# Kernel tuning notes

Hardware: AMD Instinct MI355X
Metric: run time of the kernel (lower is better)

Reference implementation:

```python
import jax, jax.numpy as jnp
import numpy as np
from functools import partial

STRIDES = (8, 16, 32)
SCORE_THRESH = 0.3
NMS_THRESH = 0.5
TOPK = 500          # fixed pre-NMS candidate count (jit-friendly substitute for boolean masking)
CLASS_OFFSET = 1e4  # offset boxes per class so cross-class IoU == 0 -> per-class NMS


def _decode(cls, reg, obj, stride):
    # cls [B,C,H,W], reg [B,4,H,W], obj [B,1,H,W]
    B, C, H, W = cls.shape
    yv, xv = jnp.meshgrid(jnp.arange(H, dtype=cls.dtype), jnp.arange(W, dtype=cls.dtype), indexing='ij')
    scores = jax.nn.sigmoid(obj) * jax.nn.sigmoid(cls)          # [B,C,H,W]
    dx, dy, dw, dh = reg[:, 0], reg[:, 1], reg[:, 2], reg[:, 3]
    cx = (xv + jax.nn.sigmoid(dx)) * stride
    cy = (yv + jax.nn.sigmoid(dy)) * stride
    w = jnp.exp(dw) * stride
    h = jnp.exp(dh) * stride
    boxes = jnp.stack([cx - w / 2, cy - h / 2, cx + w / 2, cy + h / 2], axis=-1)  # [B,H,W,4]
    return boxes.reshape(B, H * W, 4), scores.reshape(B, C, H * W).transpose(0, 2, 1)


def _pairwise_iou(boxes):
    # boxes [B,K,4] xyxy -> iou [B,K,K]
    area = (boxes[..., 2] - boxes[..., 0]) * (boxes[..., 3] - boxes[..., 1])
    x1 = jnp.maximum(boxes[:, :, None, 0], boxes[:, None, :, 0])
    y1 = jnp.maximum(boxes[:, :, None, 1], boxes[:, None, :, 1])
    x2 = jnp.minimum(boxes[:, :, None, 2], boxes[:, None, :, 2])
    y2 = jnp.minimum(boxes[:, :, None, 3], boxes[:, None, :, 3])
    inter = jnp.clip(x2 - x1, 0) * jnp.clip(y2 - y1, 0)
    union = area[:, :, None] + area[:, None, :] - inter
    return inter / (union + 1e-7)


def _greedy_nms(iou, valid):
    # iou [B,K,K], valid [B,K] -> keep [B,K]; greedy over score-sorted order (axis 1)
    B, K = valid.shape
    def step(supp, i):
        keep_i = valid[:, i] & ~supp[:, i]                    # [B]
        supp = supp | (keep_i[:, None] & (iou[:, i, :] >= NMS_THRESH))
        return supp, keep_i
    _, keep_t = jax.lax.scan(step, jnp.zeros((B, K), dtype=bool), jnp.arange(K))
    return keep_t.T  # [B,K]


def _predict(levels):
    boxes_l, scores_l = [], []
    for (c, r, o), s in zip(levels, STRIDES):
        b, sc = _decode(c, r, o, s)
        boxes_l.append(b)
        scores_l.append(sc)
    boxes = jnp.concatenate(boxes_l, axis=1)     # [B,N,4]
    scores = jnp.concatenate(scores_l, axis=1)   # [B,N,C]
    max_scores = scores.max(axis=-1)             # [B,N]
    labels = jnp.argmax(scores, axis=-1)         # [B,N]
    masked = jnp.where(max_scores > SCORE_THRESH, max_scores, -1.0)
    top_scores, idx = jax.lax.top_k(masked, TOPK)                         # sorted desc
    top_boxes = jnp.take_along_axis(boxes, idx[..., None], axis=1)        # [B,K,4]
    top_labels = jnp.take_along_axis(labels, idx, axis=1)                 # [B,K]
    valid = top_scores > SCORE_THRESH
    boxes_off = top_boxes + (top_labels.astype(top_boxes.dtype) * CLASS_OFFSET)[..., None]
    keep = _greedy_nms(_pairwise_iou(boxes_off), valid)                   # [B,K]
    out_boxes = jnp.where(keep[..., None], top_boxes, 0.0)
    out_scores = jnp.where(keep, top_scores, 0.0)
    return out_boxes, out_scores, top_labels, keep


def setup_inputs() -> dict:
    key = jax.random.key(0)
    ks = jax.random.split(key, 9)
    B, C = 64, 2
    shapes = {
        'cls_p3': (B, C, 160, 160), 'reg_p3': (B, 4, 160, 160), 'obj_p3': (B, 1, 160, 160),
        'cls_p4': (B, C, 80, 80),   'reg_p4': (B, 4, 80, 80),   'obj_p4': (B, 1, 80, 80),
        'cls_p5': (B, C, 40, 40),   'reg_p5': (B, 4, 40, 40),   'obj_p5': (B, 1, 40, 40),
    }
    return {name: jax.random.normal(k, shp, dtype=jnp.float32)
            for k, (name, shp) in zip(ks, shapes.items())}


def reference(cls_p3, reg_p3, obj_p3, cls_p4, reg_p4, obj_p4, cls_p5, reg_p5, obj_p5):
    levels = [(cls_p3, reg_p3, obj_p3), (cls_p4, reg_p4, obj_p4), (cls_p5, reg_p5, obj_p5)]
    return _predict(levels)
```

## Files before the change

kernel.cpp:

```cpp
#include <hip/hip_runtime.h>
#include <hip/hip_bf16.h>
#include <stdint.h>

#define NB 64
#define NA 33600
#define NK 500
#define HW3 25600
#define HW4 6400
#define HW5 1600
#define OFF4 25600
#define OFF5 32000
#define NBIN 2048
#define CAP 2048
#define NA4 8400
#define MROWS 512

typedef unsigned int u32;
typedef unsigned long long u64;

__device__ __forceinline__ float sigf(float x) { return 1.0f / (1.0f + expf(-x)); }

__device__ __forceinline__ u32 f2key(float f) {
  u32 u = __float_as_uint(f);
  return (u & 0x80000000u) ? ~u : (u | 0x80000000u);
}
__device__ __forceinline__ float key2f(u32 k) {
  u32 u = (k & 0x80000000u) ? (k ^ 0x80000000u) : ~k;
  return __uint_as_float(u);
}
__device__ __forceinline__ int bin_of(float s) {
  int b = (int)(s * 2048.0f);
  return b > 2047 ? 2047 : b;
}
__device__ __forceinline__ u32 mkkey(float o, float c0, float c1) {
  float so = sigf(o);
  float s = fmaxf(so * sigf(c0), so * sigf(c1));
  float masked = (s > 0.3f) ? s : -1.0f;
  return f2key(masked);
}

__global__ __launch_bounds__(256) void k_score(
    const float* __restrict__ cls3, const float* __restrict__ obj3,
    const float* __restrict__ cls4, const float* __restrict__ obj4,
    const float* __restrict__ cls5, const float* __restrict__ obj5,
    uint4* __restrict__ keys4)
{
  int b = blockIdx.y;
  int i4 = blockIdx.x * 256 + threadIdx.x;
  if (i4 >= NA4) return;
  const float* cls; const float* obj; int p4, HW;
  if (i4 < 6400)      { cls = cls3; obj = obj3; p4 = i4;        HW = HW3; }
  else if (i4 < 8000) { cls = cls4; obj = obj4; p4 = i4 - 6400; HW = HW4; }
  else                { cls = cls5; obj = obj5; p4 = i4 - 8000; HW = HW5; }
  float4 o  = reinterpret_cast<const float4*>(obj + (size_t)b * HW)[p4];
  float4 c0 = reinterpret_cast<const float4*>(cls + (size_t)(b * 2) * HW)[p4];
  float4 c1 = reinterpret_cast<const float4*>(cls + (size_t)(b * 2 + 1) * HW)[p4];
  uint4 kv;
  kv.x = mkkey(o.x, c0.x, c1.x);
  kv.y = mkkey(o.y, c0.y, c1.y);
  kv.z = mkkey(o.z, c0.z, c1.z);
  kv.w = mkkey(o.w, c0.w, c1.w);
  keys4[(size_t)b * NA4 + i4] = kv;
}

__global__ __launch_bounds__(1024) void k_topk(
    const u32* __restrict__ keys, int* __restrict__ ok,
    int* __restrict__ top_idx, float* __restrict__ top_score)
{
  int b = blockIdx.x, tid = threadIdx.x;
  __shared__ u32 hist[NBIN];
  __shared__ u32 part[256];
  __shared__ u64 cand[CAP];
  __shared__ u32 lcnt;
  __shared__ int sh_p;
  for (int i = tid; i < NBIN; i += 1024) hist[i] = 0;
  if (tid == 0) lcnt = 0;
  __syncthreads();

  const uint4* kb4 = reinterpret_cast<const uint4*>(keys + (size_t)b * NA);
  for (int i4 = tid; i4 < NA4; i4 += 1024) {
    uint4 kv = kb4[i4];
    u32 ks[4] = {kv.x, kv.y, kv.z, kv.w};
#pragma unroll
    for (int c = 0; c < 4; ++c) {
      float s = key2f(ks[c]);
      if (s > 0.3f) atomicAdd(&hist[bin_of(s)], 1u);
    }
  }
  __syncthreads();
  if (tid < 256) {
    u32 s8 = 0;
#pragma unroll
    for (int k = 0; k < 8; ++k) s8 += hist[tid * 8 + k];
    part[tid] = s8;
  }
  __syncthreads();
  for (int off = 1; off < 256; off <<= 1) {
    u32 add = 0;
    if (tid < 256 && tid + off < 256) add = part[tid + off];
    __syncthreads();
    if (tid < 256) part[tid] += add;
    __syncthreads();
  }
  if (tid == 0 && part[0] < NK) sh_p = -1;
  if (tid < 256) {
    u32 S = part[tid];
    u32 Snext = (tid == 255) ? 0u : part[tid + 1];
    if (S >= NK && Snext < NK) {
      u32 run = Snext;
      int p = tid * 8;
      for (int k = 7; k >= 0; --k) {
        run += hist[tid * 8 + k];
        if (run >= NK) { p = tid * 8 + k; break; }
      }
      sh_p = p;
    }
  }
  __syncthreads();
  int p = sh_p;
  if (p < 0) { if (tid == 0) ok[b] = 0; return; }
  for (int i4 = tid; i4 < NA4; i4 += 1024) {
    uint4 kv = kb4[i4];
    u32 ks[4] = {kv.x, kv.y, kv.z, kv.w};
#pragma unroll
    for (int c = 0; c < 4; ++c) {
      float s = key2f(ks[c]);
      if (s > 0.3f && bin_of(s) >= p) {
        u32 slot = atomicAdd(&lcnt, 1u);
        if (slot < CAP) cand[slot] = ((u64)ks[c] << 16) | (u32)(0xFFFF - (i4 * 4 + c));
      }
    }
  }
  __syncthreads();
  if (lcnt > CAP) { if (tid == 0) ok[b] = 0; return; }
  if (tid == 0) ok[b] = 1;
  int n = (int)lcnt;
  for (int t = tid; t < n; t += 1024) {
    u64 k = cand[t];
    int rank = 0;
    for (int j = 0; j < n; ++j) rank += (cand[j] > k) ? 1 : 0;
    if (rank < NK) {
      top_idx[b * NK + rank]   = 0xFFFF - (int)(k & 0xFFFFull);
      top_score[b * NK + rank] = key2f((u32)(k >> 16));
    }
  }
}

__global__ __launch_bounds__(1024) void k_select_fb(
    const u32* __restrict__ keys, const int* __restrict__ ok,
    int* __restrict__ top_idx, float* __restrict__ top_score)
{
  int b = blockIdx.x;
  if (ok[b]) return;
  int tid = threadIdx.x;
  __shared__ u32 hist[256];
  __shared__ u32 suf[256];
  __shared__ u64 coll[512];
  __shared__ u32 sh_R;
  __shared__ int sh_digit;
  __shared__ u32 sh_cnt;
  const u32* kb = keys + (size_t)b * NA;
  if (tid == 0) sh_cnt = 0;

  u64 prefix = 0, prefmask = 0;
  u32 R = NK;
  for (int pass = 0; pass < 6; ++pass) {
    int shift = 40 - 8 * pass;
    if (tid < 256) hist[tid] = 0;
    __syncthreads();
    for (int i = tid; i < NA; i += 1024) {
      u64 k48 = ((u64)kb[i] << 16) | (u32)(0xFFFF - i);
      if ((k48 & prefmask) == prefix)
        atomicAdd(&hist[(u32)(k48 >> shift) & 255u], 1u);
    }
    __syncthreads();
    if (tid < 256) suf[tid] = hist[tid];
    __syncthreads();
    for (int off = 1; off < 256; off <<= 1) {
      u32 add = 0;
      if (tid < 256 && tid + off < 256) add = suf[tid + off];
      __syncthreads();
      if (tid < 256) suf[tid] += add;
      __syncthreads();
    }
    if (tid < 256) {
      u32 s = suf[tid];
      u32 snext = (tid == 255) ? 0u : suf[tid + 1];
      if (s >= R && snext < R) { sh_digit = tid; sh_R = R - snext; }
    }
    __syncthreads();
    int dsel = sh_digit;
    R = sh_R;
    prefix |= ((u64)dsel) << shift;
    prefmask |= 0xFFull << shift;
    __syncthreads();
  }

  for (int i = tid; i < NA; i += 1024) {
    u64 k48 = ((u64)kb[i] << 16) | (u32)(0xFFFF - i);
    if (k48 >= prefix) {
      u32 slot = atomicAdd(&sh_cnt, 1u);
      if (slot < 512) coll[slot] = k48;
    }
  }
  __syncthreads();
  int n = (sh_cnt < (u32)NK) ? (int)sh_cnt : NK;
  if (tid < NK) { top_idx[b * NK + tid] = 0; top_score[b * NK + tid] = -1.0f; }
  __syncthreads();
  for (int t = tid; t < n; t += 1024) {
    u64 k = coll[t];
    int rank = 0;
    for (int j = 0; j < n; ++j) rank += (coll[j] > k) ? 1 : 0;
    int idx = 0xFFFF - (int)(k & 0xFFFFull);
    top_idx[b * NK + rank] = idx;
    top_score[b * NK + rank] = key2f((u32)(k >> 16));
  }
}

__global__ __launch_bounds__(256) void k_decode(
    const int* __restrict__ top_idx,
    const float* __restrict__ cls3, const float* __restrict__ obj3, const float* __restrict__ reg3,
    const float* __restrict__ cls4, const float* __restrict__ obj4, const float* __restrict__ reg4,
    const float* __restrict__ cls5, const float* __restrict__ obj5, const float* __restrict__ reg5,
    float4* __restrict__ boxes, float4* __restrict__ boxesoff,
    float* __restrict__ out_labels)
{
  int t = blockIdx.x * 256 + threadIdx.x;
  if (t >= NB * NK) return;
  int b = t / NK;
  int a = top_idx[t];
  const float *cls, *obj, *reg; int pos, HW, x, y; float stride;
  if (a < OFF4) {
    cls = cls3; obj = obj3; reg = reg3; pos = a; HW = HW3; stride = 8.0f;
    y = pos / 160; x = pos - y * 160;
  } else if (a < OFF5) {
    cls = cls4; obj = obj4; reg = reg4; pos = a - OFF4; HW = HW4; stride = 16.0f;
    y = pos / 80; x = pos - y * 80;
  } else {
    cls = cls5; obj = obj5; reg = reg5; pos = a - OFF5; HW = HW5; stride = 32.0f;
    y = pos / 40; x = pos - y * 40;
  }
  float dx = reg[(b * 4 + 0) * HW + pos];
  float dy = reg[(b * 4 + 1) * HW + pos];
  float dw = reg[(b * 4 + 2) * HW + pos];
  float dh = reg[(b * 4 + 3) * HW + pos];
  float cx = ((float)x + sigf(dx)) * stride;
  float cy = ((float)y + sigf(dy)) * stride;
  float w = expf(dw) * stride;
  float h = expf(dh) * stride;
  float x1 = cx - w * 0.5f, y1 = cy - h * 0.5f;
  float x2 = cx + w * 0.5f, y2 = cy + h * 0.5f;
  float so = sigf(obj[b * HW + pos]);
  float s0 = so * sigf(cls[(b * 2) * HW + pos]);
  float s1 = so * sigf(cls[(b * 2 + 1) * HW + pos]);
  int label = (s1 > s0) ? 1 : 0;
  float off = (float)label * 10000.0f;
  boxes[t]    = make_float4(x1, y1, x2, y2);
  boxesoff[t] = make_float4(x1 + off, y1 + off, x2 + off, y2 + off);
  out_labels[t] = (float)label;
}

__global__ __launch_bounds__(256) void k_iou(
    const float4* __restrict__ boxesoff, u64* __restrict__ mask)
{
  int t = blockIdx.x * 256 + threadIdx.x;
  if (t >= NB * NK * 8) return;
  int w = t & 7;
  int bi = t >> 3;
  int b = bi / NK;
  int i = bi - b * NK;
  float4 A = boxesoff[bi];
  float areaA = (A.z - A.x) * (A.w - A.y);
  const float4* base = boxesoff + b * NK;
  int j0 = w * 64;
  int jmax = (NK - j0 < 64) ? (NK - j0) : 64;
  u64 bits = 0;
  for (int jj = 0; jj < jmax; ++jj) {
    float4 Bx = base[j0 + jj];
    float areaB = (Bx.z - Bx.x) * (Bx.w - Bx.y);
    float ix1 = fmaxf(A.x, Bx.x);
    float iy1 = fmaxf(A.y, Bx.y);
    float ix2 = fminf(A.z, Bx.z);
    float iy2 = fminf(A.w, Bx.w);
    float iw = fmaxf(ix2 - ix1, 0.0f);
    float ih = fmaxf(iy2 - iy1, 0.0f);
    float inter = iw * ih;
    float uni = areaA + areaB - inter;
    float iou = inter / (uni + 1e-7f);
    bits |= ((u64)(iou >= 0.5f)) << jj;
  }
  mask[(size_t)b * (MROWS * 8) + (size_t)i * 8 + w] = bits;
}

__global__ __launch_bounds__(64) void k_nms(
    const u64* __restrict__ mask, const float* __restrict__ top_score,
    const float4* __restrict__ boxes,
    float* __restrict__ out_boxes, float* __restrict__ out_scores,
    float* __restrict__ out_keep)
{
  int b = blockIdx.x;
  int lane = threadIdx.x;
  const u64* mb = mask + (size_t)b * (MROWS * 8);

  u64 validw[8];
#pragma unroll
  for (int c = 0; c < 8; ++c) {
    int r = c * 64 + lane;
    float s = (r < NK) ? top_score[b * NK + r] : -1.0f;
    validw[c] = __ballot(s > 0.3f);
  }

  u64 supp[8] = {0, 0, 0, 0, 0, 0, 0, 0};
  u64 keepw[8];
  u64 row[2][8];

  {
    const u64* rp = mb + (size_t)lane * 8;
#pragma unroll
    for (int w = 0; w < 8; ++w) row[0][w] = rp[w];
  }

#pragma unroll
  for (int c = 0; c < 8; ++c) {
    const int cur = c & 1, nxt = cur ^ 1;
    if (c < 7) {
      const u64* rp = mb + (size_t)((c + 1) * 64 + lane) * 8;
#pragma unroll
      for (int w = 0; w < 8; ++w)
        if (w >= c + 1) row[nxt][w] = rp[w];
    }
    u32 rlo = (u32)row[cur][c];
    u32 rhi = (u32)(row[cur][c] >> 32);
    u64 sw = supp[c], vw = validw[c], km = 0;
#pragma unroll 4
    for (int i = 0; i < 64; ++i) {
      u64 wi = ((u64)(u32)__builtin_amdgcn_readlane(rhi, i) << 32) |
               (u64)(u32)__builtin_amdgcn_readlane(rlo, i);
      u64 bit = 1ull << i;
      if ((vw & bit) && !(sw & bit)) { sw |= wi; km |= bit; }
    }
    keepw[c] = km;
    u64 sel = ((km >> lane) & 1ull) ? ~0ull : 0ull;
#pragma unroll
    for (int w = c + 1; w < 8; ++w) {
      u64 v = row[cur][w] & sel;
#pragma unroll
      for (int off = 1; off < 64; off <<= 1)
        v |= (u64)__shfl_xor((unsigned long long)v, off, 64);
      supp[w] |= v;
    }
  }

#pragma unroll
  for (int c = 0; c < 8; ++c) {
    int r = c * 64 + lane;
    if (r < NK) {
      int kp = (int)((keepw[c] >> lane) & 1ull);
      float4 bx = boxes[b * NK + r];
      float s = top_score[b * NK + r];
      float4 ob;
      ob.x = kp ? bx.x : 0.0f;
      ob.y = kp ? bx.y : 0.0f;
      ob.z = kp ? bx.z : 0.0f;
      ob.w = kp ? bx.w : 0.0f;
      reinterpret_cast<float4*>(out_boxes)[b * NK + r] = ob;
      out_scores[b * NK + r] = kp ? s : 0.0f;
      out_keep[b * NK + r]   = kp ? 1.0f : 0.0f;
    }
  }
}

extern "C" void kernel_launch(void* const* d_in, const int* in_sizes, int n_in,
                              void* d_out, int out_size, void* d_ws, size_t ws_size,
                              hipStream_t stream) {
  const float* cls3 = (const float*)d_in[0];
  const float* reg3 = (const float*)d_in[1];
  const float* obj3 = (const float*)d_in[2];
  const float* cls4 = (const float*)d_in[3];
  const float* reg4 = (const float*)d_in[4];
  const float* obj4 = (const float*)d_in[5];
  const float* cls5 = (const float*)d_in[6];
  const float* reg5 = (const float*)d_in[7];
  const float* obj5 = (const float*)d_in[8];

  char* ws = (char*)d_ws;
  u32*    keys      = (u32*)   (ws + 0);
  int*    ok        = (int*)   (ws + 8601600);
  int*    top_idx   = (int*)   (ws + 8601856);
  float*  top_score = (float*) (ws + 8729856);
  float4* boxes     = (float4*)(ws + 8857856);
  float4* boxesoff  = (float4*)(ws + 9369856);
  u64*    mask      = (u64*)   (ws + 9881856);

  float* out        = (float*)d_out;
  float* out_boxes  = out;
  float* out_scores = out + 128000;
  float* out_labels = out + 160000;
  float* out_keep   = out + 192000;

  dim3 gscore((NA4 + 255) / 256, NB);
  k_score<<<gscore, 256, 0, stream>>>(cls3, obj3, cls4, obj4, cls5, obj5, (uint4*)keys);
  k_topk<<<NB, 1024, 0, stream>>>(keys, ok, top_idx, top_score);
  k_select_fb<<<NB, 1024, 0, stream>>>(keys, ok, top_idx, top_score);
  k_decode<<<(NB * NK + 255) / 256, 256, 0, stream>>>(top_idx,
      cls3, obj3, reg3, cls4, obj4, reg4, cls5, obj5, reg5,
      boxes, boxesoff, out_labels);
  k_iou<<<(NB * NK * 8 + 255) / 256, 256, 0, stream>>>(boxesoff, mask);
  k_nms<<<NB, 64, 0, stream>>>(mask, top_score, boxes, out_boxes, out_scores, out_keep);
}
```

Measured before the change: 106.9 us.

## Fuse top-k, fallback selection and box decode into one kernel

Merges the top-k kernel, the radix-select fallback kernel and the decode kernel into a single per-batch block. Selected indices now stay in shared memory instead of going through global memory, and the ok flag goes away. This removes two launches and their global round trips. It also fully unrolls the NMS greedy inner loop and broadcasts the suppression word with readfirstlane so it stays in scalar registers. In exchange, decode runs on only 500 threads of a 64-block grid, which gives less parallelism for that part.

```diff
diff --git a/kernel.cpp b/kernel.cpp
--- a/kernel.cpp
+++ b/kernel.cpp
@@ -37,6 +37,11 @@
   float s = fmaxf(so * sigf(c0), so * sigf(c1));
   float masked = (s > 0.3f) ? s : -1.0f;
   return f2key(masked);
+}
+__device__ __forceinline__ u64 uniform64(u64 v) {
+  u32 lo = (u32)__builtin_amdgcn_readfirstlane((int)(u32)v);
+  u32 hi = (u32)__builtin_amdgcn_readfirstlane((int)(u32)(v >> 32));
+  return ((u64)hi << 32) | lo;
 }
 
 __global__ __launch_bounds__(256) void k_score(
@@ -64,20 +69,33 @@
 }
 
 __global__ __launch_bounds__(1024) void k_topk(
-    const u32* __restrict__ keys, int* __restrict__ ok,
-    int* __restrict__ top_idx, float* __restrict__ top_score)
+    const u32* __restrict__ keys,
+    const float* __restrict__ cls3, const float* __restrict__ obj3, const float* __restrict__ reg3,
+    const float* __restrict__ cls4, const float* __restrict__ obj4, const float* __restrict__ reg4,
+    const float* __restrict__ cls5, const float* __restrict__ obj5, const float* __restrict__ reg5,
+    float* __restrict__ top_score,
+    float4* __restrict__ boxes, float4* __restrict__ boxesoff,
+    float* __restrict__ out_labels)
 {
   int b = blockIdx.x, tid = threadIdx.x;
   __shared__ u32 hist[NBIN];
   __shared__ u32 part[256];
   __shared__ u64 cand[CAP];
+  __shared__ int idx_lds[NK];
   __shared__ u32 lcnt;
   __shared__ int sh_p;
+  __shared__ u32 sh_R;
+  __shared__ int sh_digit;
+  __shared__ u32 sh_cnt;
+
   for (int i = tid; i < NBIN; i += 1024) hist[i] = 0;
-  if (tid == 0) lcnt = 0;
+  if (tid < NK) idx_lds[tid] = 0;
+  if (tid == 0) { lcnt = 0; }
   __syncthreads();
 
-  const uint4* kb4 = reinterpret_cast<const uint4*>(keys + (size_t)b * NA);
+  const u32* kb = keys + (size_t)b * NA;
+  const uint4* kb4 = reinterpret_cast<const uint4*>(kb);
+
   for (int i4 = tid; i4 < NA4; i4 += 1024) {
     uint4 kv = kb4[i4];
     u32 ks[4] = {kv.x, kv.y, kv.z, kv.w};
@@ -118,146 +136,125 @@
   }
   __syncthreads();
   int p = sh_p;
-  if (p < 0) { if (tid == 0) ok[b] = 0; return; }
-  for (int i4 = tid; i4 < NA4; i4 += 1024) {
-    uint4 kv = kb4[i4];
-    u32 ks[4] = {kv.x, kv.y, kv.z, kv.w};
-#pragma unroll
-    for (int c = 0; c < 4; ++c) {
-      float s = key2f(ks[c]);
-      if (s > 0.3f && bin_of(s) >= p) {
-        u32 slot = atomicAdd(&lcnt, 1u);
-        if (slot < CAP) cand[slot] = ((u64)ks[c] << 16) | (u32)(0xFFFF - (i4 * 4 + c));
-      }
-    }
-  }
-  __syncthreads();
-  if (lcnt > CAP) { if (tid == 0) ok[b] = 0; return; }
-  if (tid == 0) ok[b] = 1;
-  int n = (int)lcnt;
-  for (int t = tid; t < n; t += 1024) {
-    u64 k = cand[t];
-    int rank = 0;
-    for (int j = 0; j < n; ++j) rank += (cand[j] > k) ? 1 : 0;
-    if (rank < NK) {
-      top_idx[b * NK + rank]   = 0xFFFF - (int)(k & 0xFFFFull);
-      top_score[b * NK + rank] = key2f((u32)(k >> 16));
-    }
-  }
-}
-
-__global__ __launch_bounds__(1024) void k_select_fb(
-    const u32* __restrict__ keys, const int* __restrict__ ok,
-    int* __restrict__ top_idx, float* __restrict__ top_score)
-{
-  int b = blockIdx.x;
-  if (ok[b]) return;
-  int tid = threadIdx.x;
-  __shared__ u32 hist[256];
-  __shared__ u32 suf[256];
-  __shared__ u64 coll[512];
-  __shared__ u32 sh_R;
-  __shared__ int sh_digit;
-  __shared__ u32 sh_cnt;
-  const u32* kb = keys + (size_t)b * NA;
-  if (tid == 0) sh_cnt = 0;
-
-  u64 prefix = 0, prefmask = 0;
-  u32 R = NK;
-  for (int pass = 0; pass < 6; ++pass) {
-    int shift = 40 - 8 * pass;
-    if (tid < 256) hist[tid] = 0;
+  bool fail = (p < 0);
+  if (!fail) {
+    for (int i4 = tid; i4 < NA4; i4 += 1024) {
+      uint4 kv = kb4[i4];
+      u32 ks[4] = {kv.x, kv.y, kv.z, kv.w};
+#pragma unroll
+      for (int c = 0; c < 4; ++c) {
+        float s = key2f(ks[c]);
+        if (s > 0.3f && bin_of(s) >= p) {
+          u32 slot = atomicAdd(&lcnt, 1u);
+          if (slot < CAP) cand[slot] = ((u64)ks[c] << 16) | (u32)(0xFFFF - (i4 * 4 + c));
+        }
+      }
+    }
+    __syncthreads();
+    fail = (lcnt > CAP);
+  }
+
+  if (!fail) {
+    int n = (int)lcnt;
+    for (int t = tid; t < n; t += 1024) {
+      u64 k = cand[t];
+      int rank = 0;
+      for (int j = 0; j < n; ++j) rank += (cand[j] > k) ? 1 : 0;
+      if (rank < NK) {
+        idx_lds[rank] = 0xFFFF - (int)(k & 0xFFFFull);
+        top_score[b * NK + rank] = key2f((u32)(k >> 16));
+      }
+    }
+  } else {
+    u64 prefix = 0, prefmask = 0;
+    u32 R = NK;
+    for (int pass = 0; pass < 6; ++pass) {
+      int shift = 40 - 8 * pass;
+      if (tid < 256) part[tid] = 0;
+      __syncthreads();
+      for (int i = tid; i < NA; i += 1024) {
+        u64 k48 = ((u64)kb[i] << 16) | (u32)(0xFFFF - i);
+        if ((k48 & prefmask) == prefix)
+          atomicAdd(&part[(u32)(k48 >> shift) & 255u], 1u);
+      }
+      __syncthreads();
+      if (tid < 256) hist[tid] = part[tid];
+      __syncthreads();
+      for (int off = 1; off < 256; off <<= 1) {
+        u32 add = 0;
+        if (tid < 256 && tid + off < 256) add = hist[tid + off];
+        __syncthreads();
+        if (tid < 256) hist[tid] += add;
+        __syncthreads();
+      }
+      if (tid < 256) {
+        u32 s = hist[tid];
+        u32 snext = (tid == 255) ? 0u : hist[tid + 1];
+        if (s >= R && snext < R) { sh_digit = tid; sh_R = R - snext; }
+      }
+      __syncthreads();
+      prefix |= ((u64)sh_digit) << shift;
+      R = sh_R;
+      prefmask |= 0xFFull << shift;
+      __syncthreads();
+    }
+    if (tid == 0) sh_cnt = 0;
+    if (tid < NK) top_score[b * NK + tid] = -1.0f;
     __syncthreads();
     for (int i = tid; i < NA; i += 1024) {
       u64 k48 = ((u64)kb[i] << 16) | (u32)(0xFFFF - i);
-      if ((k48 & prefmask) == prefix)
-        atomicAdd(&hist[(u32)(k48 >> shift) & 255u], 1u);
+      if (k48 >= prefix) {
+        u32 slot = atomicAdd(&sh_cnt, 1u);
+        if (slot < 512) cand[slot] = k48;
+      }
     }
     __syncthreads();
-    if (tid < 256) suf[tid] = hist[tid];
-    __syncthreads();
-    for (int off = 1; off < 256; off <<= 1) {
-      u32 add = 0;
-      if (tid < 256 && tid + off < 256) add = suf[tid + off];
-      __syncthreads();
-      if (tid < 256) suf[tid] += add;
-      __syncthreads();
-    }
-    if (tid < 256) {
-      u32 s = suf[tid];
-      u32 snext = (tid == 255) ? 0u : suf[tid + 1];
-      if (s >= R && snext < R) { sh_digit = tid; sh_R = R - snext; }
-    }
-    __syncthreads();
-    int dsel = sh_digit;
-    R = sh_R;
-    prefix |= ((u64)dsel) << shift;
-    prefmask |= 0xFFull << shift;
-    __syncthreads();
-  }
-
-  for (int i = tid; i < NA; i += 1024) {
-    u64 k48 = ((u64)kb[i] << 16) | (u32)(0xFFFF - i);
-    if (k48 >= prefix) {
-      u32 slot = atomicAdd(&sh_cnt, 1u);
-      if (slot < 512) coll[slot] = k48;
+    int n = (sh_cnt < (u32)NK) ? (int)sh_cnt : NK;
+    for (int t = tid; t < n; t += 1024) {
+      u64 k = cand[t];
+      int rank = 0;
+      for (int j = 0; j < n; ++j) rank += (cand[j] > k) ? 1 : 0;
+      if (rank < NK) {
+        idx_lds[rank] = 0xFFFF - (int)(k & 0xFFFFull);
+        top_score[b * NK + rank] = key2f((u32)(k >> 16));
+      }
     }
   }
   __syncthreads();
-  int n = (sh_cnt < (u32)NK) ? (int)sh_cnt : NK;
-  if (tid < NK) { top_idx[b * NK + tid] = 0; top_score[b * NK + tid] = -1.0f; }
-  __syncthreads();
-  for (int t = tid; t < n; t += 1024) {
-    u64 k = coll[t];
-    int rank = 0;
-    for (int j = 0; j < n; ++j) rank += (coll[j] > k) ? 1 : 0;
-    int idx = 0xFFFF - (int)(k & 0xFFFFull);
-    top_idx[b * NK + rank] = idx;
-    top_score[b * NK + rank] = key2f((u32)(k >> 16));
-  }
-}
-
-__global__ __launch_bounds__(256) void k_decode(
-    const int* __restrict__ top_idx,
-    const float* __restrict__ cls3, const float* __restrict__ obj3, const float* __restrict__ reg3,
-    const float* __restrict__ cls4, const float* __restrict__ obj4, const float* __restrict__ reg4,
-    const float* __restrict__ cls5, const float* __restrict__ obj5, const float* __restrict__ reg5,
-    float4* __restrict__ boxes, float4* __restrict__ boxesoff,
-    float* __restrict__ out_labels)
-{
-  int t = blockIdx.x * 256 + threadIdx.x;
-  if (t >= NB * NK) return;
-  int b = t / NK;
-  int a = top_idx[t];
-  const float *cls, *obj, *reg; int pos, HW, x, y; float stride;
-  if (a < OFF4) {
-    cls = cls3; obj = obj3; reg = reg3; pos = a; HW = HW3; stride = 8.0f;
-    y = pos / 160; x = pos - y * 160;
-  } else if (a < OFF5) {
-    cls = cls4; obj = obj4; reg = reg4; pos = a - OFF4; HW = HW4; stride = 16.0f;
-    y = pos / 80; x = pos - y * 80;
-  } else {
-    cls = cls5; obj = obj5; reg = reg5; pos = a - OFF5; HW = HW5; stride = 32.0f;
-    y = pos / 40; x = pos - y * 40;
-  }
-  float dx = reg[(b * 4 + 0) * HW + pos];
-  float dy = reg[(b * 4 + 1) * HW + pos];
-  float dw = reg[(b * 4 + 2) * HW + pos];
-  float dh = reg[(b * 4 + 3) * HW + pos];
-  float cx = ((float)x + sigf(dx)) * stride;
-  float cy = ((float)y + sigf(dy)) * stride;
-  float w = expf(dw) * stride;
-  float h = expf(dh) * stride;
-  float x1 = cx - w * 0.5f, y1 = cy - h * 0.5f;
-  float x2 = cx + w * 0.5f, y2 = cy + h * 0.5f;
-  float so = sigf(obj[b * HW + pos]);
-  float s0 = so * sigf(cls[(b * 2) * HW + pos]);
-  float s1 = so * sigf(cls[(b * 2 + 1) * HW + pos]);
-  int label = (s1 > s0) ? 1 : 0;
-  float off = (float)label * 10000.0f;
-  boxes[t]    = make_float4(x1, y1, x2, y2);
-  boxesoff[t] = make_float4(x1 + off, y1 + off, x2 + off, y2 + off);
-  out_labels[t] = (float)label;
+
+  if (tid < NK) {
+    int a = idx_lds[tid];
+    const float *cls, *obj, *reg; int pos, HW, x, y; float stride;
+    if (a < OFF4) {
+      cls = cls3; obj = obj3; reg = reg3; pos = a; HW = HW3; stride = 8.0f;
+      y = pos / 160; x = pos - y * 160;
+    } else if (a < OFF5) {
+      cls = cls4; obj = obj4; reg = reg4; pos = a - OFF4; HW = HW4; stride = 16.0f;
+      y = pos / 80; x = pos - y * 80;
+    } else {
+      cls = cls5; obj = obj5; reg = reg5; pos = a - OFF5; HW = HW5; stride = 32.0f;
+      y = pos / 40; x = pos - y * 40;
+    }
+    float dx = reg[(b * 4 + 0) * HW + pos];
+    float dy = reg[(b * 4 + 1) * HW + pos];
+    float dw = reg[(b * 4 + 2) * HW + pos];
+    float dh = reg[(b * 4 + 3) * HW + pos];
+    float cx = ((float)x + sigf(dx)) * stride;
+    float cy = ((float)y + sigf(dy)) * stride;
+    float w = expf(dw) * stride;
+    float h = expf(dh) * stride;
+    float x1 = cx - w * 0.5f, y1 = cy - h * 0.5f;
+    float x2 = cx + w * 0.5f, y2 = cy + h * 0.5f;
+    float so = sigf(obj[b * HW + pos]);
+    float s0 = so * sigf(cls[(b * 2) * HW + pos]);
+    float s1 = so * sigf(cls[(b * 2 + 1) * HW + pos]);
+    int label = (s1 > s0) ? 1 : 0;
+    float off = (float)label * 10000.0f;
+    int t = b * NK + tid;
+    boxes[t]    = make_float4(x1, y1, x2, y2);
+    boxesoff[t] = make_float4(x1 + off, y1 + off, x2 + off, y2 + off);
+    out_labels[t] = (float)label;
+  }
 }
 
 __global__ __launch_bounds__(256) void k_iou(
@@ -332,7 +329,7 @@
     u32 rlo = (u32)row[cur][c];
     u32 rhi = (u32)(row[cur][c] >> 32);
     u64 sw = supp[c], vw = validw[c], km = 0;
-#pragma unroll 4
+#pragma unroll
     for (int i = 0; i < 64; ++i) {
       u64 wi = ((u64)(u32)__builtin_amdgcn_readlane(rhi, i) << 32) |
                (u64)(u32)__builtin_amdgcn_readlane(rlo, i);
@@ -347,7 +344,7 @@
 #pragma unroll
       for (int off = 1; off < 64; off <<= 1)
         v |= (u64)__shfl_xor((unsigned long long)v, off, 64);
-      supp[w] |= v;
+      supp[w] |= uniform64(v);
     }
   }
 
@@ -385,12 +382,10 @@
 
   char* ws = (char*)d_ws;
   u32*    keys      = (u32*)   (ws + 0);
-  int*    ok        = (int*)   (ws + 8601600);
-  int*    top_idx   = (int*)   (ws + 8601856);
-  float*  top_score = (float*) (ws + 8729856);
-  float4* boxes     = (float4*)(ws + 8857856);
-  float4* boxesoff  = (float4*)(ws + 9369856);
-  u64*    mask      = (u64*)   (ws + 9881856);
+  float*  top_score = (float*) (ws + 8601600);
+  float4* boxes     = (float4*)(ws + 8729600);
+  float4* boxesoff  = (float4*)(ws + 9241600);
+  u64*    mask      = (u64*)   (ws + 9753600);
 
   float* out        = (float*)d_out;
   float* out_boxes  = out;
@@ -400,11 +395,9 @@
 
   dim3 gscore((NA4 + 255) / 256, NB);
   k_score<<<gscore, 256, 0, stream>>>(cls3, obj3, cls4, obj4, cls5, obj5, (uint4*)keys);
-  k_topk<<<NB, 1024, 0, stream>>>(keys, ok, top_idx, top_score);
-  k_select_fb<<<NB, 1024, 0, stream>>>(keys, ok, top_idx, top_score);
-  k_decode<<<(NB * NK + 255) / 256, 256, 0, stream>>>(top_idx,
+  k_topk<<<NB, 1024, 0, stream>>>(keys,
       cls3, obj3, reg3, cls4, obj4, reg4, cls5, obj5, reg5,
-      boxes, boxesoff, out_labels);
+      top_score, boxes, boxesoff, out_labels);
   k_iou<<<(NB * NK * 8 + 255) / 256, 256, 0, stream>>>(boxesoff, mask);
   k_nms<<<NB, 64, 0, stream>>>(mask, top_score, boxes, out_boxes, out_scores, out_keep);
 }
```

Measured after the change: 97.31 us. 9.0% less time.
